# Kernel tuning notes

Measured on AMD Instinct MI355X. Metric: run time of the kernel, lower is better.

The kernel has to match this reference:

```python
import math
import jax, jax.numpy as jnp
import numpy as np

B, N, H, D = 2, 2048, 16, 64


def _build_idx_table(seq_len, is_causal=True):
    """Fused hierarchical lookup table, faithful to
    build_hierarchical_index_lookup_table. Returns int32 [seq_len, log2(N)+1].
    Entries are (node_index + 1), negated if causally masked.
    Node numbering: leaves 0..N-1, then each level's parents appended;
    parent(i) = i // 2 + seq_len.
    """
    assert seq_len & (seq_len - 1) == 0
    total_nodes = 2 * seq_len - 1
    max_valid = total_nodes - 2  # root is never a neighbor
    level_num = int(math.log2(seq_len))
    total_cols = level_num + 1
    idx = np.ones((seq_len, total_cols), dtype=np.int32)
    n_cur = np.arange(seq_len, dtype=np.int64)
    idx[:, 0] = (n_cur + 1).astype(np.int32)  # self leaf
    for lvl in range(1, total_cols):
        if lvl == 1:
            n_next = n_cur ^ 1          # sibling leaf
            pair = n_cur
        else:
            pair = n_cur // 2 + seq_len  # parent node
            n_next = pair ^ 1            # uncle node
        valid = n_next <= max_valid
        val = n_next + 1
        if is_causal:
            should_mask = (pair < n_next) & valid
            val = np.where(should_mask, -val, val)
        idx[:, lvl] = np.where(valid, val.astype(np.int32), idx[:, lvl])
        n_cur = n_next
    return idx


IDX_TABLE = _build_idx_table(N, is_causal=True)  # [N, LEVELS]


def setup_inputs() -> dict:
    key = jax.random.key(0)
    kq, kk, kv = jax.random.split(key, 3)
    Q = jax.random.normal(kq, (B, N, H, D), dtype=jnp.float32)
    K = jax.random.normal(kk, (B, N, H, D), dtype=jnp.float32)
    V = jax.random.normal(kv, (B, N, H, D), dtype=jnp.float32)
    return {"Q": Q, "K": K, "V": V}


def _build_tree(K, V, scale):
    """Build the full binary-tree node set [B, 2N-1, H, D] for K and V.
    Each parent is a 3-way attention mix of {parent-mean, child0, child1}
    (build_parent_nodes semantics: fp32 online softmax with +1e-9 in denom),
    with the same weights applied to K and V values."""
    Ks, Vs = [K], [V]
    Kc, Vc = K, V
    while Kc.shape[1] > 1:  # trace-time loop over log2(N) levels
        K0, K1 = Kc[:, 0::2], Kc[:, 1::2]
        V0, V1 = Vc[:, 0::2], Vc[:, 1::2]
        Kp0 = 0.5 * (K0 + K1)  # initial parent K (query)
        Vp0 = 0.5 * (V0 + V1)
        s_self = jnp.sum(Kp0 * Kp0, axis=-1) * scale  # [B,P,H]
        s0 = jnp.sum(Kp0 * K0, axis=-1) * scale
        s1 = jnp.sum(Kp0 * K1, axis=-1) * scale
        m = jnp.maximum(s_self, jnp.maximum(s0, s1))
        e_s, e0, e1 = jnp.exp(s_self - m), jnp.exp(s0 - m), jnp.exp(s1 - m)
        denom = e_s + e0 + e1 + 1e-9
        ws, w0, w1 = (e_s / denom)[..., None], (e0 / denom)[..., None], (e1 / denom)[..., None]
        Kc = ws * Kp0 + w0 * K0 + w1 * K1
        Vc = ws * Vp0 + w0 * V0 + w1 * V1
        Ks.append(Kc)
        Vs.append(Vc)
    return jnp.concatenate(Ks, axis=1), jnp.concatenate(Vs, axis=1)


def reference(Q, K, V):
    b, n, h, d = Q.shape
    scale = 1.0 / math.sqrt(d)
    K_all, V_all = _build_tree(K, V, scale)  # [B, 2N-1, H, D]

    raw = jnp.asarray(IDX_TABLE)             # [N, L], sign-encoded
    nbr = jnp.abs(raw) - 1                   # neighbor node indices
    masked = raw < 0                         # causal mask

    Kg = jnp.take(K_all, nbr, axis=1)        # [B, N, L, H, D]
    Vg = jnp.take(V_all, nbr, axis=1)

    scores = jnp.einsum('bnhd,bnlhd->bnhl', Q, Kg) * scale
    scores = jnp.where(masked[None, :, None, :], -jnp.inf, scores)
    w = jax.nn.softmax(scores, axis=-1)      # [B, N, H, L]
    out = jnp.einsum('bnhl,bnlhd->bnhd', w, Vg)
    return out
```

## Files before the change

### kernel.cpp

```cpp
#include <hip/hip_runtime.h>

#define NSEQ   2048
#define HEADS  16
#define DIM    64
#define BATCH  2
#define SCALE  0.125f

#define WSSLOTS 2048
#define ROWF4   (DIM / 4)
#define HSTRIDE (HEADS * ROWF4)
#define KVBYTES ((size_t)BATCH * WSSLOTS * HEADS * 256)

__device__ __forceinline__ int level_offset(int j) {
    return (j == 0) ? 0 : (2 * NSEQ - ((2 * NSEQ) >> j));
}

__device__ __forceinline__ float dot4(float4 a, float4 b) {
    return a.x * b.x + a.y * b.y + a.z * b.z + a.w * b.w;
}

template <int CTRL>
__device__ __forceinline__ float dpp_radd(float x) {
    int y = __builtin_amdgcn_update_dpp(0, __float_as_int(x), CTRL, 0xF, 0xF, true);
    return x + __int_as_float(y);
}
__device__ __forceinline__ float rsum16(float x) {
    x = dpp_radd<0xB1>(x);
    x = dpp_radd<0x4E>(x);
    x = dpp_radd<0x141>(x);
    x = dpp_radd<0x140>(x);
    return x;
}

__device__ __forceinline__ unsigned short bf16rne(float x) {
    unsigned u = __float_as_uint(x);
    return (unsigned short)((u + 0x7FFFu + ((u >> 16) & 1u)) >> 16);
}
__device__ __forceinline__ unsigned pack2(float a, float b) {
    return (unsigned)bf16rne(a) | ((unsigned)bf16rne(b) << 16);
}
__device__ __forceinline__ uint4 packKV(float4 k, float4 v) {
    return make_uint4(pack2(k.x, k.y), pack2(k.z, k.w),
                      pack2(v.x, v.y), pack2(v.z, v.w));
}
__device__ __forceinline__ float2 unpack2(unsigned u) {
    return make_float2(__uint_as_float(u << 16),
                       __uint_as_float(u & 0xFFFF0000u));
}
__device__ __forceinline__ float4 unpackK(uint4 p) {
    float2 a = unpack2(p.x), b = unpack2(p.y);
    return make_float4(a.x, a.y, b.x, b.y);
}
__device__ __forceinline__ float4 unpackV(uint4 p) {
    float2 a = unpack2(p.z), b = unpack2(p.w);
    return make_float4(a.x, a.y, b.x, b.y);
}

__device__ __forceinline__ void reduce3_16(float& a, float& b, float& c) {
    a = rsum16(a);
    b = rsum16(b);
    c = rsum16(c);
}

__device__ __forceinline__ void reduce6_16(float& a, float& b, float& c,
                                           float& d, float& e, float& f) {
    a = rsum16(a);
    b = rsum16(b);
    c = rsum16(c);
    d = rsum16(d);
    e = rsum16(e);
    f = rsum16(f);
}

__device__ __forceinline__ void make_parent4(float4 k0, float4 k1, float4 v0, float4 v1,
                                             float4& kc, float4& vc) {
    float4 kp, vp;
    kp.x = 0.5f * (k0.x + k1.x); kp.y = 0.5f * (k0.y + k1.y);
    kp.z = 0.5f * (k0.z + k1.z); kp.w = 0.5f * (k0.w + k1.w);
    vp.x = 0.5f * (v0.x + v1.x); vp.y = 0.5f * (v0.y + v1.y);
    vp.z = 0.5f * (v0.z + v1.z); vp.w = 0.5f * (v0.w + v1.w);
    float ss = dot4(kp, kp), sa = dot4(kp, k0), sb = dot4(kp, k1);
    reduce3_16(ss, sa, sb);
    ss *= SCALE; sa *= SCALE; sb *= SCALE;
    float mx = fmaxf(ss, fmaxf(sa, sb));
    float es = __expf(ss - mx), ea = __expf(sa - mx), eb = __expf(sb - mx);
    float inv = 1.0f / (es + ea + eb + 1e-9f);
    es *= inv; ea *= inv; eb *= inv;
    kc.x = es * kp.x + ea * k0.x + eb * k1.x;
    kc.y = es * kp.y + ea * k0.y + eb * k1.y;
    kc.z = es * kp.z + ea * k0.z + eb * k1.z;
    kc.w = es * kp.w + ea * k0.w + eb * k1.w;
    vc.x = es * vp.x + ea * v0.x + eb * v1.x;
    vc.y = es * vp.y + ea * v0.y + eb * v1.y;
    vc.z = es * vp.z + ea * v0.z + eb * v1.z;
    vc.w = es * vp.w + ea * v0.w + eb * v1.w;
}

__device__ __forceinline__ void make_parent_pair4(const float4* k, const float4* v,
                                                  float4& ka, float4& va,
                                                  float4& kb, float4& vb) {
    float4 kpa, vpa, kpb, vpb;
    kpa.x = 0.5f * (k[0].x + k[1].x); kpa.y = 0.5f * (k[0].y + k[1].y);
    kpa.z = 0.5f * (k[0].z + k[1].z); kpa.w = 0.5f * (k[0].w + k[1].w);
    vpa.x = 0.5f * (v[0].x + v[1].x); vpa.y = 0.5f * (v[0].y + v[1].y);
    vpa.z = 0.5f * (v[0].z + v[1].z); vpa.w = 0.5f * (v[0].w + v[1].w);
    kpb.x = 0.5f * (k[2].x + k[3].x); kpb.y = 0.5f * (k[2].y + k[3].y);
    kpb.z = 0.5f * (k[2].z + k[3].z); kpb.w = 0.5f * (k[2].w + k[3].w);
    vpb.x = 0.5f * (v[2].x + v[3].x); vpb.y = 0.5f * (v[2].y + v[3].y);
    vpb.z = 0.5f * (v[2].z + v[3].z); vpb.w = 0.5f * (v[2].w + v[3].w);
    float ssa = dot4(kpa, kpa), saa = dot4(kpa, k[0]), sba = dot4(kpa, k[1]);
    float ssb = dot4(kpb, kpb), sab = dot4(kpb, k[2]), sbb = dot4(kpb, k[3]);
    reduce6_16(ssa, saa, sba, ssb, sab, sbb);
    ssa *= SCALE; saa *= SCALE; sba *= SCALE;
    ssb *= SCALE; sab *= SCALE; sbb *= SCALE;
    float mxa = fmaxf(ssa, fmaxf(saa, sba));
    float mxb = fmaxf(ssb, fmaxf(sab, sbb));
    float esa = __expf(ssa - mxa), eaa = __expf(saa - mxa), eba = __expf(sba - mxa);
    float esb = __expf(ssb - mxb), eab = __expf(sab - mxb), ebb = __expf(sbb - mxb);
    float iva = 1.0f / (esa + eaa + eba + 1e-9f);
    float ivb = 1.0f / (esb + eab + ebb + 1e-9f);
    esa *= iva; eaa *= iva; eba *= iva;
    esb *= ivb; eab *= ivb; ebb *= ivb;
    ka.x = esa * kpa.x + eaa * k[0].x + eba * k[1].x;
    ka.y = esa * kpa.y + eaa * k[0].y + eba * k[1].y;
    ka.z = esa * kpa.z + eaa * k[0].z + eba * k[1].z;
    ka.w = esa * kpa.w + eaa * k[0].w + eba * k[1].w;
    va.x = esa * vpa.x + eaa * v[0].x + eba * v[1].x;
    va.y = esa * vpa.y + eaa * v[0].y + eba * v[1].y;
    va.z = esa * vpa.z + eaa * v[0].z + eba * v[1].z;
    va.w = esa * vpa.w + eaa * v[0].w + eba * v[1].w;
    kb.x = esb * kpb.x + eab * k[2].x + ebb * k[3].x;
    kb.y = esb * kpb.y + eab * k[2].y + ebb * k[3].y;
    kb.z = esb * kpb.z + eab * k[2].z + ebb * k[3].z;
    kb.w = esb * kpb.w + eab * k[2].w + ebb * k[3].w;
    vb.x = esb * vpb.x + eab * v[2].x + ebb * v[3].x;
    vb.y = esb * vpb.y + eab * v[2].y + ebb * v[3].y;
    vb.z = esb * vpb.z + eab * v[2].z + ebb * v[3].z;
    vb.w = esb * vpb.w + eab * v[2].w + ebb * v[3].w;
}

__device__ __forceinline__ void quad_step(const float4* k, const float4* v,
                                          uint4* KVw,
                                          size_t pRow0, size_t gRow,
                                          int t,
                                          float4& kg, float4& vg) {
    float4 ka, va, kb, vb;
    make_parent_pair4(k, v, ka, va, kb, vb);
    KVw[pRow0 + t] = packKV(ka, va);
    KVw[pRow0 + HSTRIDE + t] = packKV(kb, vb);
    make_parent4(ka, kb, va, vb, kg, vg);
    KVw[gRow + t] = packKV(kg, vg);
}

__global__ __launch_bounds__(256) void tree_low(const float* __restrict__ K,
                                                const float* __restrict__ V,
                                                uint4* __restrict__ KVw,
                                                float* __restrict__ Kw6,
                                                float* __restrict__ Vw6) {
    __shared__ float4 Kb[20 * ROWF4];
    __shared__ float4 Vb[20 * ROWF4];
    const float4* K4 = (const float4*)K;
    const float4* V4 = (const float4*)V;
    float4* Kw6f = (float4*)Kw6;
    float4* Vw6f = (float4*)Vw6;

    int bid = blockIdx.x;
    int c = bid & 31;
    int h = (bid >> 5) & 15;
    int b = bid >> 9;
    int lane = threadIdx.x & 63;
    int gg = (threadIdx.x >> 6) * 4 + (lane >> 4);
    int t = lane & 15;

    size_t wsBase = (size_t)(b * WSSLOTS) * HSTRIDE + h * ROWF4;

    {
        int n0 = c * 64 + 4 * gg;
        const float4* Kr = K4 + ((size_t)((b * NSEQ + n0) * HEADS + h)) * ROWF4;
        const float4* Vr = V4 + ((size_t)((b * NSEQ + n0) * HEADS + h)) * ROWF4;
        float4 k[4], v[4];
#pragma unroll
        for (int j = 0; j < 4; ++j) { k[j] = Kr[j * HSTRIDE + t]; v[j] = Vr[j * HSTRIDE + t]; }
        int s1 = c * 32 + 2 * gg;
        int s2 = 1024 + c * 16 + gg;
        float4 kg, vg;
        quad_step(k, v, KVw, wsBase + (size_t)s1 * HSTRIDE,
                  wsBase + (size_t)s2 * HSTRIDE, t, kg, vg);
        Kb[gg * ROWF4 + t] = kg;  Vb[gg * ROWF4 + t] = vg;
    }
    __syncthreads();
    if (gg < 4) {
        float4 k[4], v[4];
#pragma unroll
        for (int j = 0; j < 4; ++j) {
            k[j] = Kb[(4 * gg + j) * ROWF4 + t];
            v[j] = Vb[(4 * gg + j) * ROWF4 + t];
        }
        int s3 = 1536 + c * 8 + 2 * gg;
        int s4 = 1792 + c * 4 + gg;
        float4 kg, vg;
        quad_step(k, v, KVw, wsBase + (size_t)s3 * HSTRIDE,
                  wsBase + (size_t)s4 * HSTRIDE, t, kg, vg);
        Kb[(16 + gg) * ROWF4 + t] = kg;  Vb[(16 + gg) * ROWF4 + t] = vg;
    }
    __syncthreads();
    if (gg == 0) {
        float4 k[4], v[4];
#pragma unroll
        for (int j = 0; j < 4; ++j) {
            k[j] = Kb[(16 + j) * ROWF4 + t];
            v[j] = Vb[(16 + j) * ROWF4 + t];
        }
        int s5 = 1920 + c * 2;
        int s6 = 1984 + c;
        float4 kg, vg;
        quad_step(k, v, KVw, wsBase + (size_t)s5 * HSTRIDE,
                  wsBase + (size_t)s6 * HSTRIDE, t, kg, vg);
        size_t st = ((size_t)((b * 32 + c) * HEADS + h)) * ROWF4 + t;
        Kw6f[st] = kg;  Vw6f[st] = vg;
    }
}

__global__ __launch_bounds__(256) void tree_top(uint4* __restrict__ KVw,
                                                const float* __restrict__ Kw6,
                                                const float* __restrict__ Vw6) {
    __shared__ float4 Kb[8 * ROWF4];
    __shared__ float4 Vb[8 * ROWF4];
    const float4* Kw6f = (const float4*)Kw6;
    const float4* Vw6f = (const float4*)Vw6;

    int h = blockIdx.x & 15, b = blockIdx.x >> 4;
    int lane = threadIdx.x & 63;
    int gg = (threadIdx.x >> 6) * 4 + (lane >> 4);
    int t = lane & 15;
    size_t wsBase = (size_t)(b * WSSLOTS) * HSTRIDE + h * ROWF4;

    if (gg < 8) {
        float4 k[4], v[4];
#pragma unroll
        for (int j = 0; j < 4; ++j) {
            size_t r = ((size_t)((b * 32 + 4 * gg + j) * HEADS + h)) * ROWF4 + t;
            k[j] = Kw6f[r]; v[j] = Vw6f[r];
        }
        int s7 = 2016 + 2 * gg;
        int s8 = 2032 + gg;
        float4 kg, vg;
        quad_step(k, v, KVw, wsBase + (size_t)s7 * HSTRIDE,
                  wsBase + (size_t)s8 * HSTRIDE, t, kg, vg);
        Kb[gg * ROWF4 + t] = kg;  Vb[gg * ROWF4 + t] = vg;
    }
    __syncthreads();
    if (gg < 2) {
        float4 k[4], v[4];
#pragma unroll
        for (int j = 0; j < 4; ++j) {
            k[j] = Kb[(4 * gg + j) * ROWF4 + t];
            v[j] = Vb[(4 * gg + j) * ROWF4 + t];
        }
        int s9  = 2040 + 2 * gg;
        int s10 = 2044 + gg;
        float4 kg, vg;
        quad_step(k, v, KVw, wsBase + (size_t)s9 * HSTRIDE,
                  wsBase + (size_t)s10 * HSTRIDE, t, kg, vg);
    }
}

__global__ __launch_bounds__(256) void attn(const float* __restrict__ Q,
                                            const float* __restrict__ K,
                                            const float* __restrict__ V,
                                            const uint4* __restrict__ KVw,
                                            float* __restrict__ out) {
    const float4* Q4 = (const float4*)Q;
    const float4* K4 = (const float4*)K;
    const float4* V4 = (const float4*)V;
    float4* O4 = (float4*)out;

    int bid = blockIdx.x;
    int vbid = ((bid & 7) << 9) | (bid >> 3);
    int w = vbid * 4 + (threadIdx.x >> 6);
    int lane = threadIdx.x & 63;
    int g2 = lane >> 5;
    int hh = (lane >> 4) & 1;
    int t = lane & 15;
    int hp = w & 7;
    int p  = (w >> 3) & 1023;
    int b  = w >> 13;
    int n  = 2 * p + g2;
    int h  = 2 * hp + hh;

    int row0 = (b * NSEQ + n) * HSTRIDE;
    int rowt[10];
#pragma unroll
    for (int l = 2; l < 12; ++l) {
        int j = l - 1;
        int slot = level_offset(j) - NSEQ + ((n >> j) ^ 1);
        rowt[l - 2] = (b * WSSLOTS + slot) * HSTRIDE;
    }
    int hoff = h * ROWF4 + t;

    unsigned active = 1u | (((unsigned)p & 0x3FFu) << 2);
    active = (unsigned)__builtin_amdgcn_readfirstlane((int)active);

    float4 q4 = Q4[row0 + hoff];
    q4.x *= SCALE; q4.y *= SCALE; q4.z *= SCALE; q4.w *= SCALE;

    float4 k0 = K4[row0 + hoff];
    float4 v0 = V4[row0 + hoff];
    uint4 kv[10];
#pragma unroll
    for (int l = 2; l < 12; ++l)
        if (active & (1u << l)) kv[l - 2] = KVw[rowt[l - 2] + hoff];

    float4 ks, vs;
    ks.x = __shfl_xor(k0.x, 32, 64); ks.y = __shfl_xor(k0.y, 32, 64);
    ks.z = __shfl_xor(k0.z, 32, 64); ks.w = __shfl_xor(k0.w, 32, 64);
    vs.x = __shfl_xor(v0.x, 32, 64); vs.y = __shfl_xor(v0.y, 32, 64);
    vs.z = __shfl_xor(v0.z, 32, 64); vs.w = __shfl_xor(v0.w, 32, 64);

    float s[12];
    s[0] = dot4(q4, k0);
    s[1] = dot4(q4, ks);
#pragma unroll
    for (int l = 2; l < 12; ++l)
        s[l] = (active & (1u << l)) ? dot4(q4, unpackK(kv[l - 2])) : 0.f;

    s[0] = rsum16(s[0]);
    s[1] = rsum16(s[1]);
#pragma unroll
    for (int l = 2; l < 12; ++l)
        if (active & (1u << l)) s[l] = rsum16(s[l]);

    float mx = s[0];
    mx = fmaxf(mx, g2 ? s[1] : -3.402823466e+38f);
#pragma unroll
    for (int l = 2; l < 12; ++l)
        if (active & (1u << l)) mx = fmaxf(mx, s[l]);

    float sum;
    {
        float e0 = __expf(s[0] - mx);
        float e1 = __expf(s[1] - mx);
        e1 = g2 ? e1 : 0.f;
        s[0] = e0; s[1] = e1;
        sum = e0 + e1;
    }
#pragma unroll
    for (int l = 2; l < 12; ++l) {
        float e = (active & (1u << l)) ? __expf(s[l] - mx) : 0.f;
        s[l] = e;
        sum += e;
    }
    float inv = 1.0f / sum;

    float4 o;
    o.x = s[0] * v0.x + s[1] * vs.x;
    o.y = s[0] * v0.y + s[1] * vs.y;
    o.z = s[0] * v0.z + s[1] * vs.z;
    o.w = s[0] * v0.w + s[1] * vs.w;
#pragma unroll
    for (int l = 2; l < 12; ++l) {
        if (active & (1u << l)) {
            float4 vv = unpackV(kv[l - 2]);
            o.x += s[l] * vv.x; o.y += s[l] * vv.y;
            o.z += s[l] * vv.z; o.w += s[l] * vv.w;
        }
    }
    O4[row0 + hoff] = make_float4(o.x * inv, o.y * inv, o.z * inv, o.w * inv);
}

extern "C" void kernel_launch(void* const* d_in, const int* in_sizes, int n_in,
                              void* d_out, int out_size, void* d_ws, size_t ws_size,
                              hipStream_t stream) {
    const float* Q = (const float*)d_in[0];
    const float* K = (const float*)d_in[1];
    const float* V = (const float*)d_in[2];
    float* out = (float*)d_out;
    uint4* KVw = (uint4*)d_ws;
    float* Kw6 = (float*)((char*)d_ws + KVBYTES);
    float* Vw6 = Kw6 + (size_t)BATCH * 32 * HEADS * DIM;

    tree_low<<<1024, 256, 0, stream>>>(K, V, KVw, Kw6, Vw6);
    tree_top<<<BATCH * HEADS, 256, 0, stream>>>(KVw, Kw6, Vw6);
    attn<<<(BATCH * (NSEQ / 2) * (HEADS / 2)) / 4, 256, 0, stream>>>(Q, K, V, KVw, out);
}
```

Baseline: 110.0 us.

## Recompute level-1 tree nodes in attention kernel via LDS exchange instead of workspace

The tree builder no longer writes the level-1 parent nodes to the workspace. The attention kernel instead recomputes each pair's parent from its own K/V leaves and the shuffled sibling, then exchanges it with the neighbouring warp through shared memory to get the uncle node at level 2. Block-to-work mapping is changed so adjacent warps handle adjacent pairs for the same head. This removes one workspace level of global writes and reads, at the cost of a block-wide barrier and some extra arithmetic, and it uses full fp32 for that level instead of the packed format.

Result: no change. 108.3 us, median of 2 (-1.5%).

```diff
diff --git a/kernel.cpp b/kernel.cpp
--- a/kernel.cpp
+++ b/kernel.cpp
@@ -152,6 +152,15 @@
     KVw[gRow + t] = packKV(kg, vg);
 }
 
+__device__ __forceinline__ void quad_step_g(const float4* k, const float4* v,
+                                            uint4* KVw, size_t gRow, int t,
+                                            float4& kg, float4& vg) {
+    float4 ka, va, kb, vb;
+    make_parent_pair4(k, v, ka, va, kb, vb);
+    make_parent4(ka, kb, va, vb, kg, vg);
+    KVw[gRow + t] = packKV(kg, vg);
+}
+
 __global__ __launch_bounds__(256) void tree_low(const float* __restrict__ K,
                                                 const float* __restrict__ V,
                                                 uint4* __restrict__ KVw,
@@ -181,11 +190,9 @@
         float4 k[4], v[4];
 #pragma unroll
         for (int j = 0; j < 4; ++j) { k[j] = Kr[j * HSTRIDE + t]; v[j] = Vr[j * HSTRIDE + t]; }
-        int s1 = c * 32 + 2 * gg;
         int s2 = 1024 + c * 16 + gg;
         float4 kg, vg;
-        quad_step(k, v, KVw, wsBase + (size_t)s1 * HSTRIDE,
-                  wsBase + (size_t)s2 * HSTRIDE, t, kg, vg);
+        quad_step_g(k, v, KVw, wsBase + (size_t)s2 * HSTRIDE, t, kg, vg);
         Kb[gg * ROWF4 + t] = kg;  Vb[gg * ROWF4 + t] = vg;
     }
     __syncthreads();
@@ -270,6 +277,8 @@
                                             const float* __restrict__ V,
                                             const uint4* __restrict__ KVw,
                                             float* __restrict__ out) {
+    __shared__ float4 PK[4][2][16];
+    __shared__ float4 PV[4][2][16];
     const float4* Q4 = (const float4*)Q;
     const float4* K4 = (const float4*)K;
     const float4* V4 = (const float4*)V;
@@ -277,39 +286,39 @@
 
     int bid = blockIdx.x;
     int vbid = ((bid & 7) << 9) | (bid >> 3);
-    int w = vbid * 4 + (threadIdx.x >> 6);
+    int wid = threadIdx.x >> 6;
     int lane = threadIdx.x & 63;
     int g2 = lane >> 5;
     int hh = (lane >> 4) & 1;
     int t = lane & 15;
-    int hp = w & 7;
-    int p  = (w >> 3) & 1023;
-    int b  = w >> 13;
+    int Qd = vbid & 255;
+    int hp = (vbid >> 8) & 7;
+    int b  = vbid >> 11;
+    int p  = 4 * Qd + wid;
     int n  = 2 * p + g2;
     int h  = 2 * hp + hh;
 
     int row0 = (b * NSEQ + n) * HSTRIDE;
-    int rowt[10];
-#pragma unroll
-    for (int l = 2; l < 12; ++l) {
+    int hoff = h * ROWF4 + t;
+
+    unsigned active = 1u | (((unsigned)p & 0x3FFu) << 2);
+    active = (unsigned)__builtin_amdgcn_readfirstlane((int)active);
+
+    int rowt[9];
+#pragma unroll
+    for (int l = 3; l < 12; ++l) {
         int j = l - 1;
         int slot = level_offset(j) - NSEQ + ((n >> j) ^ 1);
-        rowt[l - 2] = (b * WSSLOTS + slot) * HSTRIDE;
-    }
-    int hoff = h * ROWF4 + t;
-
-    unsigned active = 1u | (((unsigned)p & 0x3FFu) << 2);
-    active = (unsigned)__builtin_amdgcn_readfirstlane((int)active);
+        rowt[l - 3] = (b * WSSLOTS + slot) * HSTRIDE;
+    }
 
     float4 q4 = Q4[row0 + hoff];
-    q4.x *= SCALE; q4.y *= SCALE; q4.z *= SCALE; q4.w *= SCALE;
-
     float4 k0 = K4[row0 + hoff];
     float4 v0 = V4[row0 + hoff];
-    uint4 kv[10];
-#pragma unroll
-    for (int l = 2; l < 12; ++l)
-        if (active & (1u << l)) kv[l - 2] = KVw[rowt[l - 2] + hoff];
+    uint4 kv[9];
+#pragma unroll
+    for (int l = 3; l < 12; ++l)
+        if (active & (1u << l)) kv[l - 3] = KVw[rowt[l - 3] + hoff];
 
     float4 ks, vs;
     ks.x = __shfl_xor(k0.x, 32, 64); ks.y = __shfl_xor(k0.y, 32, 64);
@@ -317,21 +326,33 @@
     vs.x = __shfl_xor(v0.x, 32, 64); vs.y = __shfl_xor(v0.y, 32, 64);
     vs.z = __shfl_xor(v0.z, 32, 64); vs.w = __shfl_xor(v0.w, 32, 64);
 
+    float4 kp1, vp1;
+    make_parent4(k0, ks, v0, vs, kp1, vp1);
+    if (lane < 32) { PK[wid][hh][t] = kp1; PV[wid][hh][t] = vp1; }
+    __syncthreads();
+    float4 kc2 = PK[wid ^ 1][hh][t];
+    float4 vc2 = PV[wid ^ 1][hh][t];
+
+    q4.x *= SCALE; q4.y *= SCALE; q4.z *= SCALE; q4.w *= SCALE;
+
     float s[12];
     s[0] = dot4(q4, k0);
     s[1] = dot4(q4, ks);
-#pragma unroll
-    for (int l = 2; l < 12; ++l)
-        s[l] = (active & (1u << l)) ? dot4(q4, unpackK(kv[l - 2])) : 0.f;
+    s[2] = (active & 4u) ? dot4(q4, kc2) : 0.f;
+#pragma unroll
+    for (int l = 3; l < 12; ++l)
+        s[l] = (active & (1u << l)) ? dot4(q4, unpackK(kv[l - 3])) : 0.f;
 
     s[0] = rsum16(s[0]);
     s[1] = rsum16(s[1]);
-#pragma unroll
-    for (int l = 2; l < 12; ++l)
+    if (active & 4u) s[2] = rsum16(s[2]);
+#pragma unroll
+    for (int l = 3; l < 12; ++l)
         if (active & (1u << l)) s[l] = rsum16(s[l]);
 
+    const float NEG = -3.402823466e+38f;
     float mx = s[0];
-    mx = fmaxf(mx, g2 ? s[1] : -3.402823466e+38f);
+    mx = fmaxf(mx, g2 ? s[1] : NEG);
 #pragma unroll
     for (int l = 2; l < 12; ++l)
         if (active & (1u << l)) mx = fmaxf(mx, s[l]);
@@ -353,14 +374,14 @@
     float inv = 1.0f / sum;
 
     float4 o;
-    o.x = s[0] * v0.x + s[1] * vs.x;
-    o.y = s[0] * v0.y + s[1] * vs.y;
-    o.z = s[0] * v0.z + s[1] * vs.z;
-    o.w = s[0] * v0.w + s[1] * vs.w;
-#pragma unroll
-    for (int l = 2; l < 12; ++l) {
+    o.x = s[0] * v0.x + s[1] * vs.x + s[2] * vc2.x;
+    o.y = s[0] * v0.y + s[1] * vs.y + s[2] * vc2.y;
+    o.z = s[0] * v0.z + s[1] * vs.z + s[2] * vc2.z;
+    o.w = s[0] * v0.w + s[1] * vs.w + s[2] * vc2.w;
+#pragma unroll
+    for (int l = 3; l < 12; ++l) {
         if (active & (1u << l)) {
-            float4 vv = unpackV(kv[l - 2]);
+            float4 vv = unpackV(kv[l - 3]);
             o.x += s[l] * vv.x; o.y += s[l] * vv.y;
             o.z += s[l] * vv.z; o.w += s[l] * vv.w;
         }
```
